# Optimization experiments

Measured on AMD Instinct MI355X. Metric: run time of the kernel, lower is better.

The kernel has to match this reference:

```python
import jax, jax.numpy as jnp
import numpy as np

CLIP_MAX = 1.0 / 1e-06  # torch.clip(1/d, max=1/1e-6)


def setup_inputs() -> dict:
    key = jax.random.key(0)
    k1, k2 = jax.random.split(key)
    base_features = jax.random.normal(k1, (4096, 512), dtype=jnp.float32)
    target_features = jax.random.normal(k2, (8192, 512), dtype=jnp.float32)
    return {"base_features": base_features, "target_features": target_features}


def _pairwise_euclidean(x, y):
    # Same math as sqrt(sum((x[:,None,:]-y[None,:,:])**2, -1)) but computed
    # via the expanded form to avoid materializing the (N,M,D) intermediate.
    x2 = jnp.sum(x * x, axis=1, keepdims=True)          # [N,1]
    y2 = jnp.sum(y * y, axis=1, keepdims=True).T        # [1,M]
    xy = x @ y.T                                        # [N,M]
    sq = jnp.maximum(x2 + y2 - 2.0 * xy, 0.0)
    return jnp.sqrt(sq)


def reference(base_features, target_features):
    # distance == 'euclidean' branch of SimilarityCalculatorFeatureOnly.forward
    dist = _pairwise_euclidean(base_features, target_features)   # [N,M]
    similarity = jnp.minimum(1.0 / dist, CLIP_MAX)                # clip at 1e6
    return (base_features, similarity)
```

## Files before the change

### kernel.cpp

```cpp
#include <hip/hip_runtime.h>
#include <hip/hip_bf16.h>
#include <stdint.h>

typedef short bf16x8 __attribute__((ext_vector_type(8)));
typedef float f32x4 __attribute__((ext_vector_type(4)));

#define D  512
#define NB 4096
#define NT 8192

__device__ __forceinline__ unsigned short f2bf(float f) {
    __hip_bfloat16 h = __float2bfloat16(f);
    return *reinterpret_cast<unsigned short*>(&h);
}

__global__ __launch_bounds__(256) void prep_kernel(
    const float* __restrict__ x, const float* __restrict__ y,
    unsigned short* __restrict__ xb, unsigned short* __restrict__ yb,
    float* __restrict__ x2, float* __restrict__ y2, float* __restrict__ copy)
{
    const int grow = blockIdx.x * 4 + (threadIdx.x >> 6);
    const int lane = threadIdx.x & 63;
    const bool isX = grow < NB;
    const int row  = isX ? grow : grow - NB;
    const float* src = isX ? x : y;
    unsigned short* dst = isX ? xb : yb;
    float* norms = isX ? x2 : y2;

    const float4* rp = reinterpret_cast<const float4*>(src + (size_t)row * D);
    float4 v0 = rp[lane * 2];
    float4 v1 = rp[lane * 2 + 1];
    if (isX) {
        float4* cp = reinterpret_cast<float4*>(copy + (size_t)row * D);
        cp[lane * 2]     = v0;
        cp[lane * 2 + 1] = v1;
    }
    float s = v0.x*v0.x + v0.y*v0.y + v0.z*v0.z + v0.w*v0.w
            + v1.x*v1.x + v1.y*v1.y + v1.z*v1.z + v1.w*v1.w;
    union { unsigned short h[8]; int4 v; } u;
    u.h[0] = f2bf(v0.x); u.h[1] = f2bf(v0.y); u.h[2] = f2bf(v0.z); u.h[3] = f2bf(v0.w);
    u.h[4] = f2bf(v1.x); u.h[5] = f2bf(v1.y); u.h[6] = f2bf(v1.z); u.h[7] = f2bf(v1.w);
    reinterpret_cast<int4*>(dst + (size_t)row * D)[lane] = u.v;
    #pragma unroll
    for (int off = 32; off > 0; off >>= 1) s += __shfl_xor(s, off);
    if (lane == 0) norms[row] = s;
}

__global__ __launch_bounds__(256, 2) void gemm_sim_kernel(
    const unsigned short* __restrict__ X, const unsigned short* __restrict__ Y,
    const float* __restrict__ x2, const float* __restrict__ y2,
    float* __restrict__ out)
{
    __shared__ alignas(16) unsigned short lds[24576];

    const int t    = threadIdx.x;
    const int lane = t & 63;
    const int w    = t >> 6;

    const int bid = blockIdx.x;
    const int xcd = bid & 7;
    const int idx = bid >> 3;
    const int rowBase = ((xcd & 3) * 8 + (idx & 7)) * 128;
    const int colBase = ((xcd >> 2) * 16 + (idx >> 3)) * 256;

    const int swz = ((t & 3) ^ ((t >> 3) & 3)) * 8;
    const unsigned short* gA = X + (size_t)(rowBase + (t >> 2)) * D + swz;
    const unsigned short* gB = Y + (size_t)(colBase + (t >> 2)) * D + swz;

    const int cread = ((lane >> 4) ^ ((lane >> 1) & 3)) * 8;
    const int aoff = (lane & 15) * 32 + cread;
    const int boff = 4096 + (w * 64 + (lane & 15)) * 32 + cread;

    f32x4 acc[8][4] = {};
    bf16x8 bfr[4];

#define STAGE_A(BUF, KT) do { \
    _Pragma("unroll") \
    for (int L = 0; L < 2; ++L) \
        __builtin_amdgcn_global_load_lds( \
            (const __attribute__((address_space(1))) void*)(gA + (size_t)L * 64 * D + (KT) * 32), \
            (__attribute__((address_space(3))) void*)(lds + (BUF) * 12288 + t * 8 + L * 2048), 16, 0, 0); \
} while (0)

#define STAGE_B(BUF, KT) do { \
    _Pragma("unroll") \
    for (int L = 0; L < 4; ++L) \
        __builtin_amdgcn_global_load_lds( \
            (const __attribute__((address_space(1))) void*)(gB + (size_t)L * 64 * D + (KT) * 32), \
            (__attribute__((address_space(3))) void*)(lds + (BUF) * 12288 + 4096 + t * 8 + L * 2048), 16, 0, 0); \
} while (0)

#define PHASE(BUF, MH, STG, CKPT) do { \
    bf16x8 _a[4]; \
    if ((MH) == 0) { \
        _Pragma("unroll") \
        for (int n = 0; n < 4; ++n) \
            bfr[n] = *(const bf16x8*)(lds + (BUF) * 12288 + boff + n * 512); \
    } \
    _Pragma("unroll") \
    for (int m = 0; m < 4; ++m) \
        _a[m] = *(const bf16x8*)(lds + (BUF) * 12288 + aoff + (MH) * 2048 + m * 512); \
    STG; \
    __builtin_amdgcn_s_barrier(); \
    asm volatile("s_waitcnt lgkmcnt(0)" ::: "memory"); \
    __builtin_amdgcn_s_setprio(1); \
    _Pragma("unroll") \
    for (int m = 0; m < 4; ++m) { \
        _Pragma("unroll") \
        for (int n = 0; n < 4; ++n) \
            acc[(MH) * 4 + m][n] = __builtin_amdgcn_mfma_f32_16x16x32_bf16(_a[m], bfr[n], acc[(MH) * 4 + m][n], 0, 0, 0); \
    } \
    __builtin_amdgcn_s_setprio(0); \
    CKPT; \
    __builtin_amdgcn_s_barrier(); \
} while (0)

    STAGE_B(0, 0); STAGE_A(0, 0); STAGE_B(1, 1);
    asm volatile("s_waitcnt vmcnt(4)" ::: "memory");
    __builtin_amdgcn_s_barrier();

#pragma unroll
    for (int j = 0; j < 8; ++j) {
        PHASE(0, 0, STAGE_A(1, 2 * j + 1), ((void)0));
        PHASE(0, 1, if (j < 7) STAGE_B(0, 2 * j + 2),
              if (j < 7) { asm volatile("s_waitcnt vmcnt(4)" ::: "memory"); }
              else       { asm volatile("s_waitcnt vmcnt(0)" ::: "memory"); });
        PHASE(1, 0, if (j < 7) STAGE_A(0, 2 * j + 2), ((void)0));
        PHASE(1, 1, if (j < 7) STAGE_B(1, 2 * j + 3),
              if (j < 7) { asm volatile("s_waitcnt vmcnt(4)" ::: "memory"); });
    }
#undef PHASE
#undef STAGE_A
#undef STAGE_B

    const int col0 = colBase + w * 64 + (lane & 15);
    const int row0 = rowBase + ((lane >> 4) << 2);
    #pragma unroll
    for (int mi = 0; mi < 8; ++mi) {
        const int rbase = row0 + (mi >> 2) * 64 + (mi & 3) * 16;
        #pragma unroll
        for (int q = 0; q < 4; ++q) {
            const int grow = rbase + q;
            const float xn = x2[grow];
            float* orow = out + (size_t)grow * NT;
            #pragma unroll
            for (int n = 0; n < 4; ++n) {
                const int gcol = col0 + n * 16;
                float sq = fmaxf(xn + y2[gcol] - 2.0f * acc[mi][n][q], 0.0f);
                orow[gcol] = fminf(rsqrtf(sq), 1.0e6f);
            }
        }
    }
}

extern "C" void kernel_launch(void* const* d_in, const int* in_sizes, int n_in,
                              void* d_out, int out_size, void* d_ws, size_t ws_size,
                              hipStream_t stream)
{
    const float* x = (const float*)d_in[0];
    const float* y = (const float*)d_in[1];
    float* out = (float*)d_out;
    char* ws = (char*)d_ws;

    unsigned short* xb = (unsigned short*)ws;
    unsigned short* yb = (unsigned short*)(ws + (4u << 20));
    float* x2 = (float*)(ws + (12u << 20));
    float* y2 = (float*)(ws + (12u << 20) + 4 * NB);

    prep_kernel<<<(NB + NT) / 4, 256, 0, stream>>>(x, y, xb, yb, x2, y2, out);
    gemm_sim_kernel<<<1024, 256, 0, stream>>>(xb, yb, x2, y2, out + (size_t)NB * D);
}
```

Measured before the change: 62.11 us.

## Make GEMM blocks persistent over four column tiles, overlapping epilogue stores with MFMA

Each block now computes a 128x512 output strip as four successive 128x128 tiles, using a 2x2 wave layout and a three-stage LDS ring over a flattened 64-step K loop. The epilogue results of each finished tile are held in registers and written out a few values per step during the next tile's MFMA work, hiding the large output-store traffic behind compute. Norms are preloaded into registers once, and the grid is halved to 512 blocks. The cost is more registers (acc plus sim arrays) and lower occupancy or parallelism, which may limit latency hiding.

```diff
diff --git a/kernel.cpp b/kernel.cpp
--- a/kernel.cpp
+++ b/kernel.cpp
@@ -56,100 +56,114 @@
     const int t    = threadIdx.x;
     const int lane = t & 63;
     const int w    = t >> 6;
+    const int wr   = w >> 1;
+    const int wc   = w & 1;
 
     const int bid = blockIdx.x;
     const int xcd = bid & 7;
     const int idx = bid >> 3;
-    const int rowBase = ((xcd & 3) * 8 + (idx & 7)) * 128;
-    const int colBase = ((xcd >> 2) * 16 + (idx >> 3)) * 256;
+    const int rowBase = ((xcd & 1) * 16 + (idx & 15)) * 128;
+    const int colBase = ((xcd >> 1) * 4 + (idx >> 4)) * 512;
 
     const int swz = ((t & 3) ^ ((t >> 3) & 3)) * 8;
     const unsigned short* gA = X + (size_t)(rowBase + (t >> 2)) * D + swz;
     const unsigned short* gB = Y + (size_t)(colBase + (t >> 2)) * D + swz;
 
     const int cread = ((lane >> 4) ^ ((lane >> 1) & 3)) * 8;
-    const int aoff = (lane & 15) * 32 + cread;
-    const int boff = 4096 + (w * 64 + (lane & 15)) * 32 + cread;
+    const int aoff = (wr * 64 + (lane & 15)) * 32 + cread;
+    const int boff = 4096 + (wc * 64 + (lane & 15)) * 32 + cread;
 
-    f32x4 acc[8][4] = {};
-    bf16x8 bfr[4];
+    float x2v[16], y2v[16];
+    {
+        const int r0 = rowBase + wr * 64 + ((lane >> 4) << 2);
+        #pragma unroll
+        for (int m = 0; m < 4; ++m)
+            #pragma unroll
+            for (int q = 0; q < 4; ++q)
+                x2v[m * 4 + q] = x2[r0 + m * 16 + q];
+        const int c0 = colBase + wc * 64 + (lane & 15);
+        #pragma unroll
+        for (int tl = 0; tl < 4; ++tl)
+            #pragma unroll
+            for (int n = 0; n < 4; ++n)
+                y2v[tl * 4 + n] = y2[c0 + tl * 128 + n * 16];
+    }
+    float* outBase = out + (size_t)(rowBase + wr * 64 + ((lane >> 4) << 2)) * NT
+                   + colBase + wc * 64 + (lane & 15);
 
-#define STAGE_A(BUF, KT) do { \
-    _Pragma("unroll") \
-    for (int L = 0; L < 2; ++L) \
-        __builtin_amdgcn_global_load_lds( \
-            (const __attribute__((address_space(1))) void*)(gA + (size_t)L * 64 * D + (KT) * 32), \
-            (__attribute__((address_space(3))) void*)(lds + (BUF) * 12288 + t * 8 + L * 2048), 16, 0, 0); \
+    f32x4 acc[4][4] = {};
+    f32x4 sim[4][4];
+    bf16x8 a[4], b[4];
+
+#define GLD(SRC, DST) __builtin_amdgcn_global_load_lds( \
+    (const __attribute__((address_space(1))) void*)(SRC), \
+    (__attribute__((address_space(3))) void*)(DST), 16, 0, 0)
+
+#define STAGE(S) do { \
+    GLD(gA + ((S) & 15) * 32,                           lds + ((S) % 3) * 8192 + t * 8); \
+    GLD(gA + ((S) & 15) * 32 + 64 * D,                  lds + ((S) % 3) * 8192 + t * 8 + 2048); \
+    GLD(gB + (size_t)((S) >> 4) * 128 * D + ((S) & 15) * 32,          lds + ((S) % 3) * 8192 + 4096 + t * 8); \
+    GLD(gB + (size_t)((S) >> 4) * 128 * D + ((S) & 15) * 32 + 64 * D, lds + ((S) % 3) * 8192 + 4096 + t * 8 + 2048); \
 } while (0)
 
-#define STAGE_B(BUF, KT) do { \
+#define BODY(G) do { \
     _Pragma("unroll") \
-    for (int L = 0; L < 4; ++L) \
-        __builtin_amdgcn_global_load_lds( \
-            (const __attribute__((address_space(1))) void*)(gB + (size_t)L * 64 * D + (KT) * 32), \
-            (__attribute__((address_space(3))) void*)(lds + (BUF) * 12288 + 4096 + t * 8 + L * 2048), 16, 0, 0); \
-} while (0)
-
-#define PHASE(BUF, MH, STG, CKPT) do { \
-    bf16x8 _a[4]; \
-    if ((MH) == 0) { \
-        _Pragma("unroll") \
-        for (int n = 0; n < 4; ++n) \
-            bfr[n] = *(const bf16x8*)(lds + (BUF) * 12288 + boff + n * 512); \
-    } \
+    for (int m = 0; m < 4; ++m) a[m] = *(const bf16x8*)(lds + ((G) % 3) * 8192 + aoff + m * 512); \
     _Pragma("unroll") \
-    for (int m = 0; m < 4; ++m) \
-        _a[m] = *(const bf16x8*)(lds + (BUF) * 12288 + aoff + (MH) * 2048 + m * 512); \
-    STG; \
+    for (int n = 0; n < 4; ++n) b[n] = *(const bf16x8*)(lds + ((G) % 3) * 8192 + boff + n * 512); \
+    if ((G) + 2 <= 63) STAGE((G) + 2); \
     __builtin_amdgcn_s_barrier(); \
     asm volatile("s_waitcnt lgkmcnt(0)" ::: "memory"); \
     __builtin_amdgcn_s_setprio(1); \
     _Pragma("unroll") \
-    for (int m = 0; m < 4; ++m) { \
+    for (int m = 0; m < 4; ++m) \
         _Pragma("unroll") \
         for (int n = 0; n < 4; ++n) \
-            acc[(MH) * 4 + m][n] = __builtin_amdgcn_mfma_f32_16x16x32_bf16(_a[m], bfr[n], acc[(MH) * 4 + m][n], 0, 0, 0); \
+            acc[m][n] = __builtin_amdgcn_mfma_f32_16x16x32_bf16(a[m], b[n], acc[m][n], 0, 0, 0); \
+    __builtin_amdgcn_s_setprio(0); \
+    if ((G) >= 16) { \
+        _Pragma("unroll") \
+        for (int i = 0; i < 4; ++i) { \
+            const int si = ((G) & 15) * 4 + i; \
+            const int mi = si >> 4, q = (si >> 2) & 3, n = si & 3; \
+            outBase[(size_t)(mi * 16 + q) * NT + (((G) >> 4) - 1) * 128 + n * 16] = sim[mi][n][q]; \
+        } \
     } \
-    __builtin_amdgcn_s_setprio(0); \
-    CKPT; \
-    __builtin_amdgcn_s_barrier(); \
+    if (((G) & 15) == 15) { \
+        _Pragma("unroll") \
+        for (int m = 0; m < 4; ++m) \
+            _Pragma("unroll") \
+            for (int n = 0; n < 4; ++n) { \
+                _Pragma("unroll") \
+                for (int q = 0; q < 4; ++q) { \
+                    float sq = fmaxf(x2v[m * 4 + q] + y2v[((G) >> 4) * 4 + n] - 2.0f * acc[m][n][q], 0.0f); \
+                    sim[m][n][q] = fminf(rsqrtf(sq), 1.0e6f); \
+                } \
+                acc[m][n] = (f32x4){0.f, 0.f, 0.f, 0.f}; \
+            } \
+    } \
+    if ((G) <= 15)      { asm volatile("s_waitcnt vmcnt(4)" ::: "memory"); } \
+    else if ((G) <= 62) { asm volatile("s_waitcnt vmcnt(8)" ::: "memory"); } \
+    if ((G) < 63) __builtin_amdgcn_s_barrier(); \
 } while (0)
 
-    STAGE_B(0, 0); STAGE_A(0, 0); STAGE_B(1, 1);
+    STAGE(0); STAGE(1);
     asm volatile("s_waitcnt vmcnt(4)" ::: "memory");
     __builtin_amdgcn_s_barrier();
 
-#pragma unroll
-    for (int j = 0; j < 8; ++j) {
-        PHASE(0, 0, STAGE_A(1, 2 * j + 1), ((void)0));
-        PHASE(0, 1, if (j < 7) STAGE_B(0, 2 * j + 2),
-              if (j < 7) { asm volatile("s_waitcnt vmcnt(4)" ::: "memory"); }
-              else       { asm volatile("s_waitcnt vmcnt(0)" ::: "memory"); });
-        PHASE(1, 0, if (j < 7) STAGE_A(0, 2 * j + 2), ((void)0));
-        PHASE(1, 1, if (j < 7) STAGE_B(1, 2 * j + 3),
-              if (j < 7) { asm volatile("s_waitcnt vmcnt(4)" ::: "memory"); });
-    }
-#undef PHASE
-#undef STAGE_A
-#undef STAGE_B
+#define B2(G) BODY(G); BODY((G) + 1);
+#define B8(G) B2(G) B2((G) + 2) B2((G) + 4) B2((G) + 6)
+    B8(0) B8(8) B8(16) B8(24) B8(32) B8(40) B8(48) B8(56)
+#undef B8
+#undef B2
+#undef BODY
+#undef STAGE
+#undef GLD
 
-    const int col0 = colBase + w * 64 + (lane & 15);
-    const int row0 = rowBase + ((lane >> 4) << 2);
     #pragma unroll
-    for (int mi = 0; mi < 8; ++mi) {
-        const int rbase = row0 + (mi >> 2) * 64 + (mi & 3) * 16;
-        #pragma unroll
-        for (int q = 0; q < 4; ++q) {
-            const int grow = rbase + q;
-            const float xn = x2[grow];
-            float* orow = out + (size_t)grow * NT;
-            #pragma unroll
-            for (int n = 0; n < 4; ++n) {
-                const int gcol = col0 + n * 16;
-                float sq = fmaxf(xn + y2[gcol] - 2.0f * acc[mi][n][q], 0.0f);
-                orow[gcol] = fminf(rsqrtf(sq), 1.0e6f);
-            }
-        }
+    for (int si = 0; si < 64; ++si) {
+        const int mi = si >> 4, q = (si >> 2) & 3, n = si & 3;
+        outBase[(size_t)(mi * 16 + q) * NT + 3 * 128 + n * 16] = sim[mi][n][q];
     }
 }
 
@@ -168,5 +182,5 @@
     float* y2 = (float*)(ws + (12u << 20) + 4 * NB);
 
     prep_kernel<<<(NB + NT) / 4, 256, 0, stream>>>(x, y, xb, yb, x2, y2, out);
-    gemm_sim_kernel<<<1024, 256, 0, stream>>>(xb, yb, x2, y2, out + (size_t)NB * D);
+    gemm_sim_kernel<<<512, 256, 0, stream>>>(xb, yb, x2, y2, out + (size_t)NB * D);
 }
```

New measurement: 70.49 us. 1.13x slower.
